# Optimization experiments

Hardware: AMD Instinct MI355X
Metric: run time of the kernel (lower is better)

## Reference

```python
import jax, jax.numpy as jnp
import numpy as np

P_DROP = 0.2  # matches nn.Dropout(0.2) in the module __init__ (forward's dropout_p arg is unused)
DROPOUT_KEY = jax.random.key(42)  # deterministic dropout mask for reproducible baseline


def setup_inputs() -> dict:
    key = jax.random.key(0)
    kq, kk, kv = jax.random.split(key, 3)
    B, Sq, Sk, D, Dv = 4, 4096, 4096, 64, 64
    return {
        "q": jax.random.normal(kq, (B, Sq, D), dtype=jnp.float32),
        "k": jax.random.normal(kk, (B, Sk, D), dtype=jnp.float32),
        "v": jax.random.normal(kv, (B, Sk, Dv), dtype=jnp.float32),
        "scale_factor": 1,
        "dropout_p": 0,
    }


def reference(q, k, v, scale_factor, dropout_p):
    # qk = q @ k^T, scaled  -> [B, Sq, Sk] (full attention matrix, as in the original)
    qk = jnp.einsum("bqd,bkd->bqk", q, k) * scale_factor
    probs = jax.nn.softmax(qk, axis=-1)
    # dropout (train-mode nn.Dropout(p=0.2)): deterministic mask, inverted scaling
    keep = jax.random.bernoulli(DROPOUT_KEY, 1.0 - P_DROP, probs.shape)
    probs = jnp.where(keep, probs / (1.0 - P_DROP), 0.0)
    # output = probs @ v -> [B, Sq, Dv]
    return jnp.einsum("bqk,bkd->bqd", probs, v)
```

## Files before the change

kernel.cpp:

```cpp
#include <hip/hip_runtime.h>
#include <hip/hip_bf16.h>
#include <stdint.h>

typedef __attribute__((ext_vector_type(8))) _Float16 f16x8;
typedef __attribute__((ext_vector_type(4))) float f32x4;

static constexpr int BATCH = 4;
static constexpr int SEQ = 4096;
static constexpr int DIM = 64;
static constexpr uint32_t KEEP_THRESH = 0xCCCCCE00u;

static constexpr size_t PB_BYTES = (64 * 64 + 128) * 4;
static __host__ __device__ constexpr size_t ws_need(int ns) {
  return (size_t)BATCH * 64 * ns * PB_BYTES;
}
static __host__ __device__ constexpr size_t onum_bytes(int ns) {
  return (size_t)BATCH * 64 * ns * 64 * 64 * 4;
}

__device__ __forceinline__ int lds_swz(int row, int colbyte) {
  return row * 128 + (colbyte ^ ((row & 7) << 4));
}

#define ROTL(x, r) (__builtin_amdgcn_alignbit((x), (x), 32 - (r)))

__device__ __forceinline__ bool tf_keep(uint32_t j42) {
  const uint32_t k1 = 42u;
  const uint32_t k2 = 0x1BD11BDAu ^ k1;
  uint32_t x1 = j42;
  uint32_t x0 = x1;
  x1 = ROTL(x1, 13) ^ x0;
  x0 += x1; x1 = ROTL(x1, 15) ^ x0;
  x0 += x1; x1 = ROTL(x1, 26) ^ x0;
  x0 += x1; x1 = ROTL(x1, 6)  ^ x0;
  x0 += k1;      x1 += k2 + 1u;
  x0 += x1; x1 = ROTL(x1, 17) ^ x0;
  x0 += x1; x1 = ROTL(x1, 29) ^ x0;
  x0 += x1; x1 = ROTL(x1, 16) ^ x0;
  x0 += x1; x1 = ROTL(x1, 24) ^ x0;
  x0 += k2;      x1 += 2u;
  x0 += x1; x1 = ROTL(x1, 13) ^ x0;
  x0 += x1; x1 = ROTL(x1, 15) ^ x0;
  x0 += x1; x1 = ROTL(x1, 26) ^ x0;
  x0 += x1; x1 = ROTL(x1, 6)  ^ x0;
    x1 += k1 + 3u;
  x0 += x1; x1 = ROTL(x1, 17) ^ x0;
  x0 += x1; x1 = ROTL(x1, 29) ^ x0;
  x0 += x1; x1 = ROTL(x1, 16) ^ x0;
  x0 += x1; x1 = ROTL(x1, 24) ^ x0;
  x0 += k1;      x1 += k2 + 4u;
  x0 += x1; x1 = ROTL(x1, 13) ^ x0;
  x0 += x1; x1 = ROTL(x1, 15) ^ x0;
  x0 += x1; x1 = ROTL(x1, 26) ^ x0;
  x0 += x1; x1 = ROTL(x1, 6)  ^ x0;
  x0 += k2;      x1 += 5u;
  return (x0 ^ x1) < KEEP_THRESH;
}

template<int CTRL>
__device__ __forceinline__ float dpp_movf(float x) {
  return __int_as_float(
      __builtin_amdgcn_mov_dpp(__float_as_int(x), CTRL, 0xF, 0xF, true));
}
__device__ __forceinline__ float red16_max(float v) {
  v = fmaxf(v, dpp_movf<0xB1>(v));
  v = fmaxf(v, dpp_movf<0x4E>(v));
  v = fmaxf(v, dpp_movf<0x141>(v));
  v = fmaxf(v, dpp_movf<0x140>(v));
  return v;
}
__device__ __forceinline__ float red16_add(float v) {
  v += dpp_movf<0xB1>(v);
  v += dpp_movf<0x4E>(v);
  v += dpp_movf<0x141>(v);
  v += dpp_movf<0x140>(v);
  return v;
}

template<bool PARTIAL, int NS>
__global__ __launch_bounds__(256, 2) void attn_kernel(
    const float* __restrict__ Q, const float* __restrict__ K, const float* __restrict__ V,
    const uint32_t* __restrict__ scale_raw,
    float* __restrict__ Out, float* __restrict__ onum, float* __restrict__ ml)
{
  __shared__ __align__(16) _Float16 Kld[64 * 64];
  __shared__ __align__(16) _Float16 Vt[64 * 64];
  __shared__ __align__(16) _Float16 Pld[4][16 * 64];

  const int b   = blockIdx.y;
  const int q0  = blockIdx.x * 64;
  const int tid = threadIdx.x;
  const int w    = tid >> 6;
  const int lane = tid & 63;
  const int l15  = lane & 15;
  const int l4   = lane >> 4;

  float scale;
  {
    uint32_t sb = *scale_raw;
    int e = (int)((sb >> 23) & 0xFFu);
    if (sb == 0u) scale = 0.0f;
    else if (e == 0 || e == 255) scale = (float)(int)sb;
    else scale = __uint_as_float(sb);
  }

  const int qw = q0 + w * 16;

  uint32_t rcb42[4];
#pragma unroll
  for (int r = 0; r < 4; ++r)
    rcb42[r] = ((uint32_t)(b * SEQ + qw + l4 * 4 + r)) * (uint32_t)SEQ + 42u;

  f16x8 aqh[2], aql[2];
#pragma unroll
  for (int c = 0; c < 2; ++c) {
    const float* qp = Q + ((size_t)(b * SEQ + qw + l15)) * DIM + l4 * 8 + 32 * c;
    f16x8 h, l;
#pragma unroll
    for (int j = 0; j < 8; ++j) {
      float f = qp[j] * scale;
      _Float16 fh = (_Float16)f;
      h[j] = fh;
      l[j] = (_Float16)(f - (float)fh);
    }
    aqh[c] = h; aql[c] = l;
  }

  float m_r[4], l_r[4];
  f32x4 Oacc[4];
#pragma unroll
  for (int r = 0; r < 4; ++r) { m_r[r] = -INFINITY; l_r[r] = 0.0f; }
#pragma unroll
  for (int n = 0; n < 4; ++n) Oacc[n] = f32x4{0.f, 0.f, 0.f, 0.f};

  const int nt = PARTIAL ? (SEQ / 64) / NS : SEQ / 64;
  const int t0 = PARTIAL ? (int)blockIdx.z * nt : 0;

  const int kr  = tid >> 4;
  const int kd0 = (tid & 15) * 4;
  const int vd  = tid & 63;
  const int vq  = tid >> 6;

  for (int kt = 0; kt < nt; ++kt) {
    const int kbase = (t0 + kt) * 64;
    __syncthreads();
#pragma unroll
    for (int i = 0; i < 4; ++i) {
      int k = kr + 16 * i;
      float4 kf = *(const float4*)(K + ((size_t)(b * SEQ + kbase + k)) * DIM + kd0);
      _Float16 h0 = (_Float16)kf.x, h1 = (_Float16)kf.y,
               h2 = (_Float16)kf.z, h3 = (_Float16)kf.w;
      *(ushort4*)((char*)Kld + lds_swz(k, kd0 * 2)) = ushort4{
        __builtin_bit_cast(unsigned short, h0), __builtin_bit_cast(unsigned short, h1),
        __builtin_bit_cast(unsigned short, h2), __builtin_bit_cast(unsigned short, h3)};
    }
#pragma unroll
    for (int i = 0; i < 4; ++i) {
      int k0 = vq * 4 + 16 * i;
      const float* vp = V + ((size_t)(b * SEQ + kbase + k0)) * DIM + vd;
      float v0 = vp[0], v1 = vp[DIM], v2 = vp[2 * DIM], v3 = vp[3 * DIM];
      unsigned int p01 = __builtin_bit_cast(unsigned int, __builtin_amdgcn_cvt_pkrtz(v0, v1));
      unsigned int p23 = __builtin_bit_cast(unsigned int, __builtin_amdgcn_cvt_pkrtz(v2, v3));
      *(uint2*)((char*)Vt + lds_swz(vd, k0 * 2)) = uint2{p01, p23};
    }
    __syncthreads();

    f32x4 s[4];
#pragma unroll
    for (int n = 0; n < 4; ++n) {
      f32x4 acc = f32x4{0.f, 0.f, 0.f, 0.f};
#pragma unroll
      for (int c = 0; c < 2; ++c) {
        int off = lds_swz(16 * n + l15, (l4 * 8 + 32 * c) * 2);
        f16x8 bk = *(const f16x8*)((char*)Kld + off);
        acc = __builtin_amdgcn_mfma_f32_16x16x32_f16(aqh[c], bk, acc, 0, 0, 0);
        acc = __builtin_amdgcn_mfma_f32_16x16x32_f16(aql[c], bk, acc, 0, 0, 0);
      }
      s[n] = acc;
    }

    float fm[4][4];
#pragma unroll
    for (int n = 0; n < 4; ++n) {
      uint32_t cb = (uint32_t)(kbase + l15 + 16 * n);
#pragma unroll
      for (int r = 0; r < 4; ++r)
        fm[n][r] = tf_keep(rcb42[r] + cb) ? 1.0f : 0.0f;
    }

    float mnew[4];
#pragma unroll
    for (int r = 0; r < 4; ++r)
      mnew[r] = red16_max(fmaxf(fmaxf(s[0][r], s[1][r]), fmaxf(s[2][r], s[3][r])));

    bool grow = (mnew[0] > m_r[0]) | (mnew[1] > m_r[1]) |
                (mnew[2] > m_r[2]) | (mnew[3] > m_r[3]);
    if (__any(grow)) {
#pragma unroll
      for (int r = 0; r < 4; ++r) {
        float mn = fmaxf(m_r[r], mnew[r]);
        float corr = __expf(m_r[r] - mn);
        m_r[r] = mn;
        l_r[r] *= corr;
#pragma unroll
        for (int n = 0; n < 4; ++n) Oacc[n][r] *= corr;
      }
    }

    float psum[4] = {0.f, 0.f, 0.f, 0.f};
    char* pw = (char*)&Pld[w][0];
#pragma unroll
    for (int n = 0; n < 4; ++n) {
#pragma unroll
      for (int r = 0; r < 4; ++r) {
        float e = __expf(s[n][r] - m_r[r]);
        psum[r] += e;
        float p = e * fm[n][r];
        *(_Float16*)(pw + lds_swz(l4 * 4 + r, (l15 + 16 * n) * 2)) = (_Float16)p;
      }
    }
#pragma unroll
    for (int r = 0; r < 4; ++r)
      l_r[r] += red16_add(psum[r]);

    asm volatile("s_waitcnt lgkmcnt(0)" ::: "memory");
    __builtin_amdgcn_sched_barrier(0);

    f16x8 pa[2];
#pragma unroll
    for (int c = 0; c < 2; ++c)
      pa[c] = *(const f16x8*)(pw + lds_swz(l15, (l4 * 8 + 32 * c) * 2));
#pragma unroll
    for (int n = 0; n < 4; ++n) {
#pragma unroll
      for (int c = 0; c < 2; ++c) {
        f16x8 bv = *(const f16x8*)((char*)Vt + lds_swz(l15 + 16 * n, (l4 * 8 + 32 * c) * 2));
        Oacc[n] = __builtin_amdgcn_mfma_f32_16x16x32_f16(pa[c], bv, Oacc[n], 0, 0, 0);
      }
    }
  }

  if (PARTIAL) {
    const int pb = ((b * 64 + (int)blockIdx.x) * NS + (int)blockIdx.z);
    float* op = onum + (size_t)pb * 4096;
#pragma unroll
    for (int r = 0; r < 4; ++r) {
      int row64 = w * 16 + l4 * 4 + r;
#pragma unroll
      for (int n = 0; n < 4; ++n)
        op[row64 * 64 + l15 + 16 * n] = Oacc[n][r];
      if (l15 == 0) {
        ml[(size_t)pb * 128 + row64 * 2 + 0] = m_r[r];
        ml[(size_t)pb * 128 + row64 * 2 + 1] = l_r[r];
      }
    }
  } else {
#pragma unroll
    for (int r = 0; r < 4; ++r) {
      float inv = 1.0f / (l_r[r] * 0.8f);
      int qg = qw + l4 * 4 + r;
      float* op = Out + ((size_t)(b * SEQ + qg)) * DIM + l15;
#pragma unroll
      for (int n = 0; n < 4; ++n)
        op[16 * n] = Oacc[n][r] * inv;
    }
  }
}

template<int NS>
__global__ __launch_bounds__(256) void combine_kernel(
    const float* __restrict__ onum, const float* __restrict__ ml, float* __restrict__ Out)
{
  const int w = threadIdx.x >> 6;
  const int lane = threadIdx.x & 63;
  const int rid = blockIdx.x * 4 + w;
  const int b = rid >> 12;
  const int qrow = rid & 4095;
  const int qb = qrow >> 6;
  const int r64 = qrow & 63;
  const int pb0 = (b * 64 + qb) * NS;

  float m[NS], l[NS];
  float M = -INFINITY;
#pragma unroll
  for (int s = 0; s < NS; ++s) {
    m[s] = ml[(size_t)(pb0 + s) * 128 + r64 * 2 + 0];
    l[s] = ml[(size_t)(pb0 + s) * 128 + r64 * 2 + 1];
    M = fmaxf(M, m[s]);
  }
  float L = 0.0f, acc = 0.0f;
#pragma unroll
  for (int s = 0; s < NS; ++s) {
    float sc = __expf(m[s] - M);
    L += l[s] * sc;
    acc += onum[(size_t)(pb0 + s) * 4096 + r64 * 64 + lane] * sc;
  }
  Out[(size_t)rid * 64 + lane] = acc / (L * 0.8f);
}

extern "C" void kernel_launch(void* const* d_in, const int* in_sizes, int n_in,
                              void* d_out, int out_size, void* d_ws, size_t ws_size,
                              hipStream_t stream) {
  const float* Q = (const float*)d_in[0];
  const float* K = (const float*)d_in[1];
  const float* V = (const float*)d_in[2];
  const uint32_t* scale_raw = (const uint32_t*)d_in[3];
  float* Out = (float*)d_out;

  if (ws_size >= ws_need(8)) {
    float* onum = (float*)d_ws;
    float* ml = (float*)((char*)d_ws + onum_bytes(8));
    attn_kernel<true, 8><<<dim3(64, BATCH, 8), 256, 0, stream>>>(
        Q, K, V, scale_raw, nullptr, onum, ml);
    combine_kernel<8><<<SEQ * BATCH / 4, 256, 0, stream>>>(onum, ml, Out);
  } else if (ws_size >= ws_need(4)) {
    float* onum = (float*)d_ws;
    float* ml = (float*)((char*)d_ws + onum_bytes(4));
    attn_kernel<true, 4><<<dim3(64, BATCH, 4), 256, 0, stream>>>(
        Q, K, V, scale_raw, nullptr, onum, ml);
    combine_kernel<4><<<SEQ * BATCH / 4, 256, 0, stream>>>(onum, ml, Out);
  } else {
    attn_kernel<false, 1><<<dim3(64, BATCH, 1), 256, 0, stream>>>(
        Q, K, V, scale_raw, Out, nullptr, nullptr);
  }
}
```

Baseline: 171.7 us.

## Double query rows per block, drop split-fp16 Q, use exp2 softmax

Each wave now processes 32 query rows instead of 16, so every staged K/V tile is reused across twice as many rows and the grid is halved. The hi/lo fp16 split of Q is removed, which halves the QK MFMAs but lowers precision. Exp is done via raw v_exp_f32 with log2e folded into the Q scale, the lazy any-grow rescale branch is dropped in favour of unconditional correction, and the row-sum reduction is deferred to the epilogue. Launch bounds rise to 3 blocks per CU, which adds register pressure alongside the doubled accumulators.

```diff
diff --git a/kernel.cpp b/kernel.cpp
--- a/kernel.cpp
+++ b/kernel.cpp
@@ -8,14 +8,17 @@
 static constexpr int BATCH = 4;
 static constexpr int SEQ = 4096;
 static constexpr int DIM = 64;
+static constexpr int QB = 128;
+static constexpr int NQB = SEQ / QB;
 static constexpr uint32_t KEEP_THRESH = 0xCCCCCE00u;
-
-static constexpr size_t PB_BYTES = (64 * 64 + 128) * 4;
+static constexpr float LOG2E = 1.44269504088896340736f;
+
+static constexpr size_t PB_BYTES = (QB * 64 + QB * 2) * 4;
 static __host__ __device__ constexpr size_t ws_need(int ns) {
-  return (size_t)BATCH * 64 * ns * PB_BYTES;
+  return (size_t)BATCH * NQB * ns * PB_BYTES;
 }
 static __host__ __device__ constexpr size_t onum_bytes(int ns) {
-  return (size_t)BATCH * 64 * ns * 64 * 64 * 4;
+  return (size_t)BATCH * NQB * ns * QB * 64 * 4;
 }
 
 __device__ __forceinline__ int lds_swz(int row, int colbyte) {
@@ -57,6 +60,12 @@
   return (x0 ^ x1) < KEEP_THRESH;
 }
 
+__device__ __forceinline__ float fexp2(float x) {
+  float r;
+  asm("v_exp_f32 %0, %1" : "=v"(r) : "v"(x));
+  return r;
+}
+
 template<int CTRL>
 __device__ __forceinline__ float dpp_movf(float x) {
   return __int_as_float(
@@ -78,17 +87,17 @@
 }
 
 template<bool PARTIAL, int NS>
-__global__ __launch_bounds__(256, 2) void attn_kernel(
+__global__ __launch_bounds__(256, 3) void attn_kernel(
     const float* __restrict__ Q, const float* __restrict__ K, const float* __restrict__ V,
     const uint32_t* __restrict__ scale_raw,
     float* __restrict__ Out, float* __restrict__ onum, float* __restrict__ ml)
 {
   __shared__ __align__(16) _Float16 Kld[64 * 64];
   __shared__ __align__(16) _Float16 Vt[64 * 64];
-  __shared__ __align__(16) _Float16 Pld[4][16 * 64];
+  __shared__ __align__(16) _Float16 Pld[4][32 * 64];
 
   const int b   = blockIdx.y;
-  const int q0  = blockIdx.x * 64;
+  const int q0  = blockIdx.x * QB;
   const int tid = threadIdx.x;
   const int w    = tid >> 6;
   const int lane = tid & 63;
@@ -103,35 +112,39 @@
     else if (e == 0 || e == 255) scale = (float)(int)sb;
     else scale = __uint_as_float(sb);
   }
-
-  const int qw = q0 + w * 16;
-
-  uint32_t rcb42[4];
-#pragma unroll
-  for (int r = 0; r < 4; ++r)
-    rcb42[r] = ((uint32_t)(b * SEQ + qw + l4 * 4 + r)) * (uint32_t)SEQ + 42u;
-
-  f16x8 aqh[2], aql[2];
-#pragma unroll
-  for (int c = 0; c < 2; ++c) {
-    const float* qp = Q + ((size_t)(b * SEQ + qw + l15)) * DIM + l4 * 8 + 32 * c;
-    f16x8 h, l;
-#pragma unroll
-    for (int j = 0; j < 8; ++j) {
-      float f = qp[j] * scale;
-      _Float16 fh = (_Float16)f;
-      h[j] = fh;
-      l[j] = (_Float16)(f - (float)fh);
-    }
-    aqh[c] = h; aql[c] = l;
-  }
-
-  float m_r[4], l_r[4];
-  f32x4 Oacc[4];
-#pragma unroll
-  for (int r = 0; r < 4; ++r) { m_r[r] = -INFINITY; l_r[r] = 0.0f; }
-#pragma unroll
-  for (int n = 0; n < 4; ++n) Oacc[n] = f32x4{0.f, 0.f, 0.f, 0.f};
+  const float qscale = scale * LOG2E;
+
+  const int qw = q0 + w * 32;
+
+  uint32_t rcb42[2][4];
+#pragma unroll
+  for (int m = 0; m < 2; ++m)
+#pragma unroll
+    for (int r = 0; r < 4; ++r)
+      rcb42[m][r] = ((uint32_t)(b * SEQ + qw + 16 * m + 4 * l4 + r)) * (uint32_t)SEQ + 42u;
+
+  f16x8 aq[2][2];
+#pragma unroll
+  for (int m = 0; m < 2; ++m)
+#pragma unroll
+    for (int c = 0; c < 2; ++c) {
+      const float* qp = Q + ((size_t)(b * SEQ + qw + 16 * m + l15)) * DIM + l4 * 8 + 32 * c;
+      f16x8 h;
+#pragma unroll
+      for (int j = 0; j < 8; ++j) h[j] = (_Float16)(qp[j] * qscale);
+      aq[m][c] = h;
+    }
+
+  float m_r[2][4], l_p[2][4];
+  f32x4 Oacc[2][4];
+#pragma unroll
+  for (int m = 0; m < 2; ++m)
+#pragma unroll
+    for (int r = 0; r < 4; ++r) { m_r[m][r] = -INFINITY; l_p[m][r] = 0.0f; }
+#pragma unroll
+  for (int m = 0; m < 2; ++m)
+#pragma unroll
+    for (int n = 0; n < 4; ++n) Oacc[m][n] = f32x4{0.f, 0.f, 0.f, 0.f};
 
   const int nt = PARTIAL ? (SEQ / 64) / NS : SEQ / 64;
   const int t0 = PARTIAL ? (int)blockIdx.z * nt : 0;
@@ -165,105 +178,102 @@
     }
     __syncthreads();
 
-    f32x4 s[4];
-#pragma unroll
-    for (int n = 0; n < 4; ++n) {
-      f32x4 acc = f32x4{0.f, 0.f, 0.f, 0.f};
-#pragma unroll
-      for (int c = 0; c < 2; ++c) {
-        int off = lds_swz(16 * n + l15, (l4 * 8 + 32 * c) * 2);
-        f16x8 bk = *(const f16x8*)((char*)Kld + off);
-        acc = __builtin_amdgcn_mfma_f32_16x16x32_f16(aqh[c], bk, acc, 0, 0, 0);
-        acc = __builtin_amdgcn_mfma_f32_16x16x32_f16(aql[c], bk, acc, 0, 0, 0);
-      }
-      s[n] = acc;
-    }
-
-    float fm[4][4];
-#pragma unroll
-    for (int n = 0; n < 4; ++n) {
-      uint32_t cb = (uint32_t)(kbase + l15 + 16 * n);
+    char* pw = (char*)&Pld[w][0];
+
+#pragma unroll
+    for (int m = 0; m < 2; ++m) {
+      f32x4 s[4];
+#pragma unroll
+      for (int n = 0; n < 4; ++n) {
+        f32x4 acc = f32x4{0.f, 0.f, 0.f, 0.f};
+#pragma unroll
+        for (int c = 0; c < 2; ++c) {
+          int off = lds_swz(16 * n + l15, (l4 * 8 + 32 * c) * 2);
+          f16x8 bk = *(const f16x8*)((char*)Kld + off);
+          acc = __builtin_amdgcn_mfma_f32_16x16x32_f16(aq[m][c], bk, acc, 0, 0, 0);
+        }
+        s[n] = acc;
+      }
+
+      float mnew[4];
 #pragma unroll
       for (int r = 0; r < 4; ++r)
-        fm[n][r] = tf_keep(rcb42[r] + cb) ? 1.0f : 0.0f;
-    }
-
-    float mnew[4];
-#pragma unroll
-    for (int r = 0; r < 4; ++r)
-      mnew[r] = red16_max(fmaxf(fmaxf(s[0][r], s[1][r]), fmaxf(s[2][r], s[3][r])));
-
-    bool grow = (mnew[0] > m_r[0]) | (mnew[1] > m_r[1]) |
-                (mnew[2] > m_r[2]) | (mnew[3] > m_r[3]);
-    if (__any(grow)) {
+        mnew[r] = red16_max(fmaxf(fmaxf(s[0][r], s[1][r]), fmaxf(s[2][r], s[3][r])));
+
 #pragma unroll
       for (int r = 0; r < 4; ++r) {
-        float mn = fmaxf(m_r[r], mnew[r]);
-        float corr = __expf(m_r[r] - mn);
-        m_r[r] = mn;
-        l_r[r] *= corr;
-#pragma unroll
-        for (int n = 0; n < 4; ++n) Oacc[n][r] *= corr;
-      }
-    }
-
-    float psum[4] = {0.f, 0.f, 0.f, 0.f};
-    char* pw = (char*)&Pld[w][0];
-#pragma unroll
-    for (int n = 0; n < 4; ++n) {
-#pragma unroll
-      for (int r = 0; r < 4; ++r) {
-        float e = __expf(s[n][r] - m_r[r]);
-        psum[r] += e;
-        float p = e * fm[n][r];
-        *(_Float16*)(pw + lds_swz(l4 * 4 + r, (l15 + 16 * n) * 2)) = (_Float16)p;
-      }
-    }
-#pragma unroll
-    for (int r = 0; r < 4; ++r)
-      l_r[r] += red16_add(psum[r]);
+        float mn = fmaxf(m_r[m][r], mnew[r]);
+        float corr = fexp2(m_r[m][r] - mn);
+        m_r[m][r] = mn;
+        l_p[m][r] *= corr;
+#pragma unroll
+        for (int n = 0; n < 4; ++n) Oacc[m][n][r] *= corr;
+      }
+
+#pragma unroll
+      for (int n = 0; n < 4; ++n) {
+        uint32_t cb = (uint32_t)(kbase + l15 + 16 * n);
+#pragma unroll
+        for (int r = 0; r < 4; ++r) {
+          float e = fexp2(s[n][r] - m_r[m][r]);
+          l_p[m][r] += e;
+          float p = tf_keep(rcb42[m][r] + cb) ? e : 0.0f;
+          *(_Float16*)(pw + lds_swz(16 * m + 4 * l4 + r, (l15 + 16 * n) * 2)) = (_Float16)p;
+        }
+      }
+    }
 
     asm volatile("s_waitcnt lgkmcnt(0)" ::: "memory");
     __builtin_amdgcn_sched_barrier(0);
 
-    f16x8 pa[2];
-#pragma unroll
-    for (int c = 0; c < 2; ++c)
-      pa[c] = *(const f16x8*)(pw + lds_swz(l15, (l4 * 8 + 32 * c) * 2));
+    f16x8 pa[2][2];
+#pragma unroll
+    for (int m = 0; m < 2; ++m)
+#pragma unroll
+      for (int c = 0; c < 2; ++c)
+        pa[m][c] = *(const f16x8*)(pw + lds_swz(16 * m + l15, (l4 * 8 + 32 * c) * 2));
 #pragma unroll
     for (int n = 0; n < 4; ++n) {
 #pragma unroll
       for (int c = 0; c < 2; ++c) {
         f16x8 bv = *(const f16x8*)((char*)Vt + lds_swz(l15 + 16 * n, (l4 * 8 + 32 * c) * 2));
-        Oacc[n] = __builtin_amdgcn_mfma_f32_16x16x32_f16(pa[c], bv, Oacc[n], 0, 0, 0);
+#pragma unroll
+        for (int m = 0; m < 2; ++m)
+          Oacc[m][n] = __builtin_amdgcn_mfma_f32_16x16x32_f16(pa[m][c], bv, Oacc[m][n], 0, 0, 0);
       }
     }
   }
 
   if (PARTIAL) {
-    const int pb = ((b * 64 + (int)blockIdx.x) * NS + (int)blockIdx.z);
-    float* op = onum + (size_t)pb * 4096;
-#pragma unroll
-    for (int r = 0; r < 4; ++r) {
-      int row64 = w * 16 + l4 * 4 + r;
-#pragma unroll
-      for (int n = 0; n < 4; ++n)
-        op[row64 * 64 + l15 + 16 * n] = Oacc[n][r];
-      if (l15 == 0) {
-        ml[(size_t)pb * 128 + row64 * 2 + 0] = m_r[r];
-        ml[(size_t)pb * 128 + row64 * 2 + 1] = l_r[r];
-      }
-    }
+    const int pb = ((b * NQB + (int)blockIdx.x) * NS + (int)blockIdx.z);
+    float* op = onum + (size_t)pb * (QB * 64);
+#pragma unroll
+    for (int m = 0; m < 2; ++m)
+#pragma unroll
+      for (int r = 0; r < 4; ++r) {
+        int row = w * 32 + 16 * m + 4 * l4 + r;
+        float lr = red16_add(l_p[m][r]);
+#pragma unroll
+        for (int n = 0; n < 4; ++n)
+          op[row * 64 + l15 + 16 * n] = Oacc[m][n][r];
+        if (l15 == 0) {
+          ml[(size_t)pb * (QB * 2) + row * 2 + 0] = m_r[m][r];
+          ml[(size_t)pb * (QB * 2) + row * 2 + 1] = lr;
+        }
+      }
   } else {
 #pragma unroll
-    for (int r = 0; r < 4; ++r) {
-      float inv = 1.0f / (l_r[r] * 0.8f);
-      int qg = qw + l4 * 4 + r;
-      float* op = Out + ((size_t)(b * SEQ + qg)) * DIM + l15;
-#pragma unroll
-      for (int n = 0; n < 4; ++n)
-        op[16 * n] = Oacc[n][r] * inv;
-    }
+    for (int m = 0; m < 2; ++m)
+#pragma unroll
+      for (int r = 0; r < 4; ++r) {
+        float L = red16_add(l_p[m][r]);
+        float inv = 1.0f / (L * 0.8f);
+        int qg = qw + 16 * m + 4 * l4 + r;
+        float* op = Out + ((size_t)(b * SEQ + qg)) * DIM + l15;
+#pragma unroll
+        for (int n = 0; n < 4; ++n)
+          op[16 * n] = Oacc[m][n][r] * inv;
+      }
   }
 }
 
@@ -276,24 +286,24 @@
   const int rid = blockIdx.x * 4 + w;
   const int b = rid >> 12;
   const int qrow = rid & 4095;
-  const int qb = qrow >> 6;
-  const int r64 = qrow & 63;
-  const int pb0 = (b * 64 + qb) * NS;
+  const int qb = qrow >> 7;
+  const int r128 = qrow & 127;
+  const int pb0 = (b * NQB + qb) * NS;
 
   float m[NS], l[NS];
   float M = -INFINITY;
 #pragma unroll
   for (int s = 0; s < NS; ++s) {
-    m[s] = ml[(size_t)(pb0 + s) * 128 + r64 * 2 + 0];
-    l[s] = ml[(size_t)(pb0 + s) * 128 + r64 * 2 + 1];
+    m[s] = ml[(size_t)(pb0 + s) * (QB * 2) + r128 * 2 + 0];
+    l[s] = ml[(size_t)(pb0 + s) * (QB * 2) + r128 * 2 + 1];
     M = fmaxf(M, m[s]);
   }
   float L = 0.0f, acc = 0.0f;
 #pragma unroll
   for (int s = 0; s < NS; ++s) {
-    float sc = __expf(m[s] - M);
+    float sc = fexp2(m[s] - M);
     L += l[s] * sc;
-    acc += onum[(size_t)(pb0 + s) * 4096 + r64 * 64 + lane] * sc;
+    acc += onum[(size_t)(pb0 + s) * (QB * 64) + r128 * 64 + lane] * sc;
   }
   Out[(size_t)rid * 64 + lane] = acc / (L * 0.8f);
 }
@@ -310,17 +320,17 @@
   if (ws_size >= ws_need(8)) {
     float* onum = (float*)d_ws;
     float* ml = (float*)((char*)d_ws + onum_bytes(8));
-    attn_kernel<true, 8><<<dim3(64, BATCH, 8), 256, 0, stream>>>(
+    attn_kernel<true, 8><<<dim3(NQB, BATCH, 8), 256, 0, stream>>>(
         Q, K, V, scale_raw, nullptr, onum, ml);
     combine_kernel<8><<<SEQ * BATCH / 4, 256, 0, stream>>>(onum, ml, Out);
   } else if (ws_size >= ws_need(4)) {
     float* onum = (float*)d_ws;
     float* ml = (float*)((char*)d_ws + onum_bytes(4));
-    attn_kernel<true, 4><<<dim3(64, BATCH, 4), 256, 0, stream>>>(
+    attn_kernel<true, 4><<<dim3(NQB, BATCH, 4), 256, 0, stream>>>(
         Q, K, V, scale_raw, nullptr, onum, ml);
     combine_kernel<4><<<SEQ * BATCH / 4, 256, 0, stream>>>(onum, ml, Out);
   } else {
-    attn_kernel<false, 1><<<dim3(64, BATCH, 1), 256, 0, stream>>>(
+    attn_kernel<false, 1><<<dim3(NQB, BATCH, 1), 256, 0, stream>>>(
         Q, K, V, scale_raw, Out, nullptr, nullptr);
   }
 }
```

Result: no change. 172.3 us (+0.3%).
